# Kernel optimization log

Hardware: AMD Instinct MI355X
Metric: run time of the kernel (lower is better)

## Reference

```python
import jax, jax.numpy as jnp
import numpy as np

B, H, M, K = 4096, 1024, 4096, 8


def setup_inputs() -> dict:
    key = jax.random.key(0)
    ks = jax.random.split(key, 9)
    s = 1.0 / np.sqrt(H)
    return {
        "a": jax.random.normal(ks[0], (B, H), dtype=jnp.float32),
        "b": jax.random.normal(ks[1], (B, H), dtype=jnp.float32),
        "memory": jax.random.normal(ks[2], (M, H), dtype=jnp.float32),
        "Wa": jax.random.uniform(ks[3], (H, H), minval=-s, maxval=s, dtype=jnp.float32),
        "ba": jax.random.uniform(ks[4], (H,), minval=-s, maxval=s, dtype=jnp.float32),
        "Wb": jax.random.uniform(ks[5], (H, H), minval=-s, maxval=s, dtype=jnp.float32),
        "bb": jax.random.uniform(ks[6], (H,), minval=-s, maxval=s, dtype=jnp.float32),
        "Wc": jax.random.uniform(ks[7], (K, 1), minval=-1.0, maxval=1.0, dtype=jnp.float32),
        "bc": jax.random.uniform(ks[8], (K,), minval=-1.0, maxval=1.0, dtype=jnp.float32),
    }


def _l2_normalize(x, eps=1e-12):
    # matches F.normalize(dim=1): x / max(||x||, eps)
    n = jnp.linalg.norm(x, axis=1, keepdims=True)
    return x / jnp.maximum(n, eps)


def reference(a, b, memory, Wa, ba, Wb, bb, Wc, bc):
    ta = a @ Wa.T + ba                      # [B, H]
    tb = b @ Wb.T + bb                      # [B, H]
    cos_a = _l2_normalize(ta) @ memory.T    # [B, M] (memory NOT normalized, as in source)
    cos_b = _l2_normalize(tb) @ memory.T    # [B, M]
    weights = jax.nn.softmax(cos_a + cos_b, axis=1)
    wm = weights @ memory                   # [B, H]
    # Linear(1, k) on [B, H, 1] then permute(0,2,1): out[b,k,h] = wm[b,h]*Wc[k,0] + bc[k]
    out = wm[:, None, :] * Wc[:, 0][None, :, None] + bc[None, :, None]  # [B, K, H]
    return out
```

## Files before the change

### kernel.cpp

```cpp
#include <hip/hip_runtime.h>
#include <stdint.h>

#define BSZ 4096
#define HDIM 1024
#define MMEM 4096
#define KOUT 8

typedef __attribute__((ext_vector_type(4))) float f32x4;
typedef __attribute__((ext_vector_type(8))) short s16x8;

__device__ __forceinline__ unsigned short f2bf(float f) {
    uint32_t u = __builtin_bit_cast(uint32_t, f);
    u += 0x7FFFu + ((u >> 16) & 1u);
    return (unsigned short)(u >> 16);
}

__global__ __launch_bounds__(256) void cvt2_f32_bf16(
    const float* __restrict__ in0, const float* __restrict__ in1,
    unsigned short* __restrict__ out, int n4) {
    int i = blockIdx.x * blockDim.x + threadIdx.x;
    if (i >= n4) return;
    const float* src = blockIdx.y ? in1 : in0;
    float4 v = reinterpret_cast<const float4*>(src)[i];
    ushort4 o;
    o.x = f2bf(v.x); o.y = f2bf(v.y); o.z = f2bf(v.z); o.w = f2bf(v.w);
    reinterpret_cast<ushort4*>(out + (size_t)blockIdx.y * n4 * 4)[i] = o;
}

__global__ __launch_bounds__(256) void transpose_cvt(
    const float* __restrict__ mem, unsigned short* __restrict__ mem_bf,
    unsigned short* __restrict__ memT, int M, int H) {
    __shared__ float tile[32][33];
    const int h0 = blockIdx.x * 32, m0 = blockIdx.y * 32;
    const int tx = threadIdx.x, ty = threadIdx.y;
#pragma unroll
    for (int j = 0; j < 4; ++j) {
        int m = m0 + ty + j * 8;
        float v = mem[(size_t)m * H + h0 + tx];
        tile[ty + j * 8][tx] = v;
        mem_bf[(size_t)m * H + h0 + tx] = f2bf(v);
    }
    __syncthreads();
#pragma unroll
    for (int j = 0; j < 4; ++j) {
        int h = h0 + ty + j * 8;
        memT[(size_t)h * M + m0 + tx] = f2bf(tile[tx][ty + j * 8]);
    }
}

template <int EPI>
__global__ __launch_bounds__(256, 2) void gemm_bt(
    const unsigned short* __restrict__ A, const unsigned short* __restrict__ Bm,
    float* __restrict__ C, unsigned short* __restrict__ Ebf,
    int N, int Kdim,
    const float* __restrict__ bias, const float* __restrict__ bias1,
    size_t zA, size_t zB, size_t zC, float* __restrict__ rowsum) {
    __shared__ alignas(16) unsigned short ldsA[4096];
    __shared__ alignas(16) unsigned short ldsB[4096];

    const int tid  = threadIdx.x;
    const int lane = tid & 63;
    const int w    = tid >> 6;
    const int wm   = w >> 1, wn = w & 1;

    const int z = blockIdx.z;
    A += (size_t)z * zA;
    Bm += (size_t)z * zB;
    C += (size_t)z * zC;
    const float* bi = (z != 0 && bias1 != nullptr) ? bias1 : bias;

    const int gx  = gridDim.x;
    const int nwg = gx * gridDim.y;
    const int lid = blockIdx.y * gx + blockIdx.x;
    const int s   = (lid & 7) * (nwg >> 3) + (lid >> 3);
    const int m0 = (s / gx) * 128, n0 = (s % gx) * 128;

    const int g0 = tid >> 6;
    const int ck = (tid >> 4) & 3;
    const int rr = tid & 15;
    size_t baseA0 = (size_t)(m0 + g0 * 16 + rr) * Kdim + ck * 8;
    size_t baseA1 = baseA0 + (size_t)64 * Kdim;
    size_t baseB0 = (size_t)(n0 + g0 * 16 + rr) * Kdim + ck * 8;
    size_t baseB1 = baseB0 + (size_t)64 * Kdim;

    char* ldsAc = (char*)ldsA;
    char* ldsBc = (char*)ldsB;
    char* dA0 = ldsAc + tid * 16;
    char* dA1 = ldsAc + 4096 + tid * 16;
    char* dB0 = ldsBc + tid * 16;
    char* dB1 = ldsBc + 4096 + tid * 16;

    f32x4 acc[4][4] = {};

    const int frOff = ((lane >> 4) * 256 + (lane & 15) * 16);

    for (int ks = 0; ks < Kdim; ks += 32) {
        __builtin_amdgcn_global_load_lds(
            (const __attribute__((address_space(1))) void*)(A + baseA0 + ks),
            (__attribute__((address_space(3))) void*)dA0, 16, 0, 0);
        __builtin_amdgcn_global_load_lds(
            (const __attribute__((address_space(1))) void*)(A + baseA1 + ks),
            (__attribute__((address_space(3))) void*)dA1, 16, 0, 0);
        __builtin_amdgcn_global_load_lds(
            (const __attribute__((address_space(1))) void*)(Bm + baseB0 + ks),
            (__attribute__((address_space(3))) void*)dB0, 16, 0, 0);
        __builtin_amdgcn_global_load_lds(
            (const __attribute__((address_space(1))) void*)(Bm + baseB1 + ks),
            (__attribute__((address_space(3))) void*)dB1, 16, 0, 0);
        __syncthreads();

        s16x8 af[4], bfv[4];
#pragma unroll
        for (int m = 0; m < 4; ++m)
            af[m] = *(const s16x8*)(ldsAc + (wm * 4 + m) * 1024 + frOff);
#pragma unroll
        for (int n = 0; n < 4; ++n)
            bfv[n] = *(const s16x8*)(ldsBc + (wn * 4 + n) * 1024 + frOff);
#pragma unroll
        for (int m = 0; m < 4; ++m)
#pragma unroll
            for (int n = 0; n < 4; ++n)
                acc[m][n] = __builtin_amdgcn_mfma_f32_16x16x32_bf16(
                    af[m], bfv[n], acc[m][n], 0, 0, 0);
        __syncthreads();
    }

    if (EPI == 1) {
#pragma unroll
        for (int m = 0; m < 4; ++m)
#pragma unroll
            for (int n = 0; n < 4; ++n) {
                int rowb = m0 + wm * 64 + m * 16 + (lane >> 4) * 4;
                int col  = n0 + wn * 64 + n * 16 + (lane & 15);
                float bv = bi[col];
#pragma unroll
                for (int r = 0; r < 4; ++r)
                    C[(size_t)(rowb + r) * N + col] = acc[m][n][r] + bv;
            }
    }

    if (EPI == 3) {
#pragma unroll
        for (int m = 0; m < 4; ++m)
#pragma unroll
            for (int n = 0; n < 4; ++n)
#pragma unroll
                for (int r = 0; r < 4; ++r)
                    acc[m][n][r] = __expf(acc[m][n][r]);
#pragma unroll
        for (int m = 0; m < 4; ++m)
#pragma unroll
            for (int n = 0; n < 4; ++n) {
                int rowb = m0 + wm * 64 + m * 16 + (lane >> 4) * 4;
                int col  = n0 + wn * 64 + n * 16 + (lane & 15);
#pragma unroll
                for (int r = 0; r < 4; ++r)
                    Ebf[(size_t)(rowb + r) * N + col] = f2bf(acc[m][n][r]);
            }
#pragma unroll
        for (int m = 0; m < 4; ++m)
#pragma unroll
            for (int r = 0; r < 4; ++r) {
                float sv = (acc[m][0][r] + acc[m][1][r]) +
                           (acc[m][2][r] + acc[m][3][r]);
                sv += __shfl_xor(sv, 1);
                sv += __shfl_xor(sv, 2);
                sv += __shfl_xor(sv, 4);
                sv += __shfl_xor(sv, 8);
                if ((lane & 15) == 0) {
                    int row = m0 + wm * 64 + m * 16 + (lane >> 4) * 4 + r;
                    atomicAdd(&rowsum[row], sv);
                }
            }
    }

    if (EPI == 4) {
        float rinv[4][4];
#pragma unroll
        for (int m = 0; m < 4; ++m)
#pragma unroll
            for (int r = 0; r < 4; ++r) {
                int row = m0 + wm * 64 + m * 16 + (lane >> 4) * 4 + r;
                rinv[m][r] = 1.0f / rowsum[row];
            }
#pragma unroll
        for (int m = 0; m < 4; ++m)
#pragma unroll
            for (int n = 0; n < 4; ++n) {
                int rowb = m0 + wm * 64 + m * 16 + (lane >> 4) * 4;
                int col  = n0 + wn * 64 + n * 16 + (lane & 15);
#pragma unroll
                for (int r = 0; r < 4; ++r)
                    C[(size_t)(rowb + r) * N + col] = acc[m][n][r] * rinv[m][r];
            }
    }
}

__global__ __launch_bounds__(256) void norm_add(
    const float* __restrict__ ta, const float* __restrict__ tb,
    unsigned short* __restrict__ u, int H) {
    const int row = blockIdx.x;
    const int tid = threadIdx.x;
    float4 va = reinterpret_cast<const float4*>(ta + (size_t)row * H)[tid];
    float4 vb = reinterpret_cast<const float4*>(tb + (size_t)row * H)[tid];
    float sa = va.x * va.x + va.y * va.y + va.z * va.z + va.w * va.w;
    float sb = vb.x * vb.x + vb.y * vb.y + vb.z * vb.z + vb.w * vb.w;
#pragma unroll
    for (int off = 32; off; off >>= 1) {
        sa += __shfl_xor(sa, off);
        sb += __shfl_xor(sb, off);
    }
    __shared__ float reda[4], redb[4];
    if ((tid & 63) == 0) { reda[tid >> 6] = sa; redb[tid >> 6] = sb; }
    __syncthreads();
    float SA = (reda[0] + reda[1]) + (reda[2] + reda[3]);
    float SB = (redb[0] + redb[1]) + (redb[2] + redb[3]);
    float ra = 1.f / fmaxf(sqrtf(SA), 1e-12f);
    float rb = 1.f / fmaxf(sqrtf(SB), 1e-12f);
    ushort4 o;
    o.x = f2bf(va.x * ra + vb.x * rb);
    o.y = f2bf(va.y * ra + vb.y * rb);
    o.z = f2bf(va.z * ra + vb.z * rb);
    o.w = f2bf(va.w * ra + vb.w * rb);
    reinterpret_cast<ushort4*>(u + (size_t)row * H)[tid] = o;
}

__global__ __launch_bounds__(256) void hub_expand(
    const float* __restrict__ wm, const float* __restrict__ Wc,
    const float* __restrict__ bc, float* __restrict__ out) {
    const int b = blockIdx.x;
    const int t = threadIdx.x;
    float4 v = reinterpret_cast<const float4*>(wm)[(size_t)b * 256 + t];
#pragma unroll
    for (int k = 0; k < KOUT; ++k) {
        float wv = Wc[k], bv = bc[k];
        float4 o;
        o.x = v.x * wv + bv; o.y = v.y * wv + bv;
        o.z = v.z * wv + bv; o.w = v.w * wv + bv;
        reinterpret_cast<float4*>(out)[((size_t)b * KOUT + k) * 256 + t] = o;
    }
}

extern "C" void kernel_launch(void* const* d_in, const int* in_sizes, int n_in,
                              void* d_out, int out_size, void* d_ws, size_t ws_size,
                              hipStream_t stream) {
    const float* a      = (const float*)d_in[0];
    const float* b      = (const float*)d_in[1];
    const float* memory = (const float*)d_in[2];
    const float* Wa     = (const float*)d_in[3];
    const float* ba     = (const float*)d_in[4];
    const float* Wb     = (const float*)d_in[5];
    const float* bb     = (const float*)d_in[6];
    const float* Wc     = (const float*)d_in[7];
    const float* bc     = (const float*)d_in[8];
    float* out = (float*)d_out;

    const int B = BSZ, H = HDIM, M = MMEM;
    char* ws = (char*)d_ws;
    const size_t MB = 1u << 20;
    unsigned short* a_bf   = (unsigned short*)(ws + 0 * MB);
    unsigned short* Wa_bf  = (unsigned short*)(ws + 16 * MB);
    unsigned short* mem_bf = (unsigned short*)(ws + 20 * MB);
    unsigned short* memT   = (unsigned short*)(ws + 28 * MB);
    float*          ta     = (float*)(ws + 36 * MB);
    unsigned short* e_bf   = (unsigned short*)(ws + 36 * MB);
    unsigned short* u_bf   = (unsigned short*)(ws + 68 * MB);
    float*          rowsum = (float*)(ws + 76 * MB);
    float*          wm     = (float*)(ws + 80 * MB);

    cvt2_f32_bf16<<<dim3(B * H / 4 / 256, 2), 256, 0, stream>>>(a, b, a_bf, B * H / 4);
    cvt2_f32_bf16<<<dim3(H * H / 4 / 256, 2), 256, 0, stream>>>(Wa, Wb, Wa_bf, H * H / 4);
    transpose_cvt<<<dim3(H / 32, M / 32), dim3(32, 8), 0, stream>>>(memory, mem_bf, memT, M, H);

    gemm_bt<1><<<dim3(H / 128, B / 128, 2), 256, 0, stream>>>(
        a_bf, Wa_bf, ta, nullptr, H, H, ba, bb,
        (size_t)B * H, (size_t)H * H, (size_t)B * H, nullptr);

    norm_add<<<B, 256, 0, stream>>>(ta, ta + (size_t)B * H, u_bf, H);

    hipMemsetAsync(rowsum, 0, (size_t)B * sizeof(float), stream);

    gemm_bt<3><<<dim3(M / 128, B / 128), 256, 0, stream>>>(
        u_bf, mem_bf, nullptr, e_bf, M, H, nullptr, nullptr, 0, 0, 0, rowsum);

    gemm_bt<4><<<dim3(H / 128, B / 128), 256, 0, stream>>>(
        e_bf, memT, wm, nullptr, H, M, nullptr, nullptr, 0, 0, 0, rowsum);

    hub_expand<<<B, 256, 0, stream>>>(wm, Wc, bc, out);
}
```

Baseline: 438.1 us.

## Split-K the projection and weighted-memory GEMMs with atomic accumulation

```diff
diff --git a/kernel.cpp b/kernel.cpp
--- a/kernel.cpp
+++ b/kernel.cpp
@@ -52,7 +52,7 @@
 __global__ __launch_bounds__(256, 2) void gemm_bt(
     const unsigned short* __restrict__ A, const unsigned short* __restrict__ Bm,
     float* __restrict__ C, unsigned short* __restrict__ Ebf,
-    int N, int Kdim,
+    int N, int Kdim, int nab,
     const float* __restrict__ bias, const float* __restrict__ bias1,
     size_t zA, size_t zB, size_t zC, float* __restrict__ rowsum) {
     __shared__ alignas(16) unsigned short ldsA[4096];
@@ -63,11 +63,15 @@
     const int w    = tid >> 6;
     const int wm   = w >> 1, wn = w & 1;
 
-    const int z = blockIdx.z;
-    A += (size_t)z * zA;
-    Bm += (size_t)z * zB;
-    C += (size_t)z * zC;
-    const float* bi = (z != 0 && bias1 != nullptr) ? bias1 : bias;
+    const int z  = blockIdx.z;
+    const int ab = z % nab;
+    const int ks = z / nab;
+    const int KSPLIT = gridDim.z / nab;
+    const int Kc = Kdim / KSPLIT;
+    A  += (size_t)ab * zA + (size_t)ks * Kc;
+    Bm += (size_t)ab * zB + (size_t)ks * Kc;
+    C  += (size_t)ab * zC;
+    const float* bi = (ab != 0 && bias1 != nullptr) ? bias1 : bias;
 
     const int gx  = gridDim.x;
     const int nwg = gx * gridDim.y;
@@ -94,18 +98,18 @@
 
     const int frOff = ((lane >> 4) * 256 + (lane & 15) * 16);
 
-    for (int ks = 0; ks < Kdim; ks += 32) {
-        __builtin_amdgcn_global_load_lds(
-            (const __attribute__((address_space(1))) void*)(A + baseA0 + ks),
+    for (int ksi = 0; ksi < Kc; ksi += 32) {
+        __builtin_amdgcn_global_load_lds(
+            (const __attribute__((address_space(1))) void*)(A + baseA0 + ksi),
             (__attribute__((address_space(3))) void*)dA0, 16, 0, 0);
         __builtin_amdgcn_global_load_lds(
-            (const __attribute__((address_space(1))) void*)(A + baseA1 + ks),
+            (const __attribute__((address_space(1))) void*)(A + baseA1 + ksi),
             (__attribute__((address_space(3))) void*)dA1, 16, 0, 0);
         __builtin_amdgcn_global_load_lds(
-            (const __attribute__((address_space(1))) void*)(Bm + baseB0 + ks),
+            (const __attribute__((address_space(1))) void*)(Bm + baseB0 + ksi),
             (__attribute__((address_space(3))) void*)dB0, 16, 0, 0);
         __builtin_amdgcn_global_load_lds(
-            (const __attribute__((address_space(1))) void*)(Bm + baseB1 + ks),
+            (const __attribute__((address_space(1))) void*)(Bm + baseB1 + ksi),
             (__attribute__((address_space(3))) void*)dB1, 16, 0, 0);
         __syncthreads();
 
@@ -132,10 +136,10 @@
             for (int n = 0; n < 4; ++n) {
                 int rowb = m0 + wm * 64 + m * 16 + (lane >> 4) * 4;
                 int col  = n0 + wn * 64 + n * 16 + (lane & 15);
-                float bv = bi[col];
-#pragma unroll
-                for (int r = 0; r < 4; ++r)
-                    C[(size_t)(rowb + r) * N + col] = acc[m][n][r] + bv;
+                float bv = (ks == 0) ? bi[col] : 0.f;
+#pragma unroll
+                for (int r = 0; r < 4; ++r)
+                    atomicAdd(&C[(size_t)(rowb + r) * N + col], acc[m][n][r] + bv);
             }
     }
 
@@ -174,15 +178,7 @@
             }
     }
 
-    if (EPI == 4) {
-        float rinv[4][4];
-#pragma unroll
-        for (int m = 0; m < 4; ++m)
-#pragma unroll
-            for (int r = 0; r < 4; ++r) {
-                int row = m0 + wm * 64 + m * 16 + (lane >> 4) * 4 + r;
-                rinv[m][r] = 1.0f / rowsum[row];
-            }
+    if (EPI == 5) {
 #pragma unroll
         for (int m = 0; m < 4; ++m)
 #pragma unroll
@@ -191,7 +187,7 @@
                 int col  = n0 + wn * 64 + n * 16 + (lane & 15);
 #pragma unroll
                 for (int r = 0; r < 4; ++r)
-                    C[(size_t)(rowb + r) * N + col] = acc[m][n][r] * rinv[m][r];
+                    atomicAdd(&C[(size_t)(rowb + r) * N + col], acc[m][n][r]);
             }
     }
 }
@@ -226,11 +222,14 @@
 }
 
 __global__ __launch_bounds__(256) void hub_expand(
-    const float* __restrict__ wm, const float* __restrict__ Wc,
-    const float* __restrict__ bc, float* __restrict__ out) {
+    const float* __restrict__ wm, const float* __restrict__ rowsum,
+    const float* __restrict__ Wc, const float* __restrict__ bc,
+    float* __restrict__ out) {
     const int b = blockIdx.x;
     const int t = threadIdx.x;
+    float rs = 1.0f / rowsum[b];
     float4 v = reinterpret_cast<const float4*>(wm)[(size_t)b * 256 + t];
+    v.x *= rs; v.y *= rs; v.z *= rs; v.w *= rs;
 #pragma unroll
     for (int k = 0; k < KOUT; ++k) {
         float wv = Wc[k], bv = bc[k];
@@ -268,23 +267,27 @@
     float*          rowsum = (float*)(ws + 76 * MB);
     float*          wm     = (float*)(ws + 80 * MB);
 
+    hipMemsetAsync(ta, 0, (size_t)2 * B * H * sizeof(float), stream);
+    hipMemsetAsync(rowsum, 0, (size_t)B * sizeof(float), stream);
+    hipMemsetAsync(wm, 0, (size_t)B * H * sizeof(float), stream);
+
     cvt2_f32_bf16<<<dim3(B * H / 4 / 256, 2), 256, 0, stream>>>(a, b, a_bf, B * H / 4);
     cvt2_f32_bf16<<<dim3(H * H / 4 / 256, 2), 256, 0, stream>>>(Wa, Wb, Wa_bf, H * H / 4);
     transpose_cvt<<<dim3(H / 32, M / 32), dim3(32, 8), 0, stream>>>(memory, mem_bf, memT, M, H);
 
-    gemm_bt<1><<<dim3(H / 128, B / 128, 2), 256, 0, stream>>>(
-        a_bf, Wa_bf, ta, nullptr, H, H, ba, bb,
+    gemm_bt<1><<<dim3(H / 128, B / 128, 4), 256, 0, stream>>>(
+        a_bf, Wa_bf, ta, nullptr, H, H, 2, ba, bb,
         (size_t)B * H, (size_t)H * H, (size_t)B * H, nullptr);
 
     norm_add<<<B, 256, 0, stream>>>(ta, ta + (size_t)B * H, u_bf, H);
 
-    hipMemsetAsync(rowsum, 0, (size_t)B * sizeof(float), stream);
-
-    gemm_bt<3><<<dim3(M / 128, B / 128), 256, 0, stream>>>(
-        u_bf, mem_bf, nullptr, e_bf, M, H, nullptr, nullptr, 0, 0, 0, rowsum);
-
-    gemm_bt<4><<<dim3(H / 128, B / 128), 256, 0, stream>>>(
-        e_bf, memT, wm, nullptr, H, M, nullptr, nullptr, 0, 0, 0, rowsum);
-
-    hub_expand<<<B, 256, 0, stream>>>(wm, Wc, bc, out);
-}
+    gemm_bt<3><<<dim3(M / 128, B / 128, 1), 256, 0, stream>>>(
+        u_bf, mem_bf, nullptr, e_bf, M, H, 1, nullptr, nullptr,
+        0, 0, 0, rowsum);
+
+    gemm_bt<5><<<dim3(H / 128, B / 128, 4), 256, 0, stream>>>(
+        e_bf, memT, wm, nullptr, H, M, 1, nullptr, nullptr,
+        0, 0, 0, nullptr);
+
+    hub_expand<<<B, 256, 0, stream>>>(wm, rowsum, Wc, bc, out);
+}
```

Result: slower. 479.5 us (+9.4%).
